# Kernel tuning notes

Hardware: AMD Instinct MI355X
Metric: run time of the kernel (lower is better)

Reference implementation:

```python
import jax, jax.numpy as jnp
import numpy as np

B, R, N, D, H, QK, K = 32, 200, 200, 128, 8, 16, 10
CLIP = 10.0  # standard POMO logit clipping


def setup_inputs() -> dict:
    key = jax.random.key(0)
    ks = jax.random.split(key, 12)
    encoded_nodes = jax.random.normal(ks[0], (B, N, D), jnp.float32)
    distance = jax.random.uniform(ks[1], (B, N, N), jnp.float32)
    current = jax.random.randint(ks[2], (B, R), 0, N)
    u = jax.random.uniform(ks[3], (B, R, N))
    ninf_mask = jnp.where(u < 0.3, -jnp.inf, 0.0).astype(jnp.float32)
    s = 0.02
    Wq = jax.random.normal(ks[4], (2 * D, H * QK), jnp.float32) * s
    Wk = jax.random.normal(ks[5], (D, H * QK), jnp.float32) * s
    Wv = jax.random.normal(ks[6], (D, H * QK), jnp.float32) * s
    Wmhc = jax.random.normal(ks[7], (H * QK, D), jnp.float32) * s
    b_mhc = jnp.zeros((D,), jnp.float32)
    W1 = jax.random.normal(ks[8], (K * D, 5 * D), jnp.float32) * s
    b1 = jnp.zeros((5 * D,), jnp.float32)
    W2 = jax.random.normal(ks[9], (5 * D, D), jnp.float32) * s
    b2 = jnp.zeros((D,), jnp.float32)
    return {"encoded_nodes": encoded_nodes, "distance": distance, "ninf_mask": ninf_mask,
            "current": current, "Wq": Wq, "Wk": Wk, "Wv": Wv, "Wmhc": Wmhc, "b_mhc": b_mhc,
            "W1": W1, "b1": b1, "W2": W2, "b2": b2}


def _search_unvisited(current, distance, ninf_mask):
    # rows of distance at current nodes: [B,R,N] (avoids B*R*N*N materialization)
    dist_f = jnp.take_along_axis(distance, current[:, :, None], axis=1)
    dist_m = jnp.where(jnp.isfinite(ninf_mask), dist_f, jnp.inf)
    neg_vals, idx = jax.lax.top_k(-dist_m, K)  # k smallest distances
    vals = -neg_vals
    return jnp.where(jnp.isinf(vals), N, idx)  # pad index N for masked-out slots


def _gather_pad0(encoded_nodes, idx):
    padded = jnp.concatenate([encoded_nodes, jnp.zeros((B, 1, D), encoded_nodes.dtype)], axis=1)
    g = jnp.take_along_axis(padded, idx.reshape(B, R * K)[:, :, None], axis=1)
    return g.reshape(B, R, K, D)


def _gather_pad_avg(a):
    # replace all-zero (pad) rows by the mean of non-zero rows within each [K,D] group
    is_zero = jnp.sum(a, axis=-1) == 0  # [B,R,K]
    cnt = jnp.maximum(jnp.sum(~is_zero, axis=-1).astype(a.dtype), 1e-9)  # [B,R]
    mean = jnp.sum(a, axis=2) / cnt[..., None]  # [B,R,D]
    return jnp.where(is_zero[..., None], mean[:, :, None, :], a)


def reference(encoded_nodes, distance, ninf_mask, current,
              Wq, Wk, Wv, Wmhc, b_mhc, W1, b1, W2, b2):
    knn = _search_unvisited(current, distance, ninf_mask)         # [B,R,K]
    a = _gather_pad0(encoded_nodes, knn)                          # [B,R,K,D]
    b = _gather_pad_avg(a)                                        # [B,R,K,D]
    h = jnp.maximum(b.reshape(B, R, K * D) @ W1 + b1, 0.0)
    unv = h @ W2 + b2                                             # [B,R,D]
    cur_emb = jnp.take_along_axis(encoded_nodes, current[:, :, None], axis=1)  # [B,R,D]
    qin = jnp.concatenate([cur_emb, unv], axis=-1)                # [B,R,2D]
    q = (qin @ Wq).reshape(B, R, H, QK).transpose(0, 2, 1, 3)     # [B,H,R,QK]
    k = (encoded_nodes @ Wk).reshape(B, N, H, QK).transpose(0, 2, 1, 3)
    v = (encoded_nodes @ Wv).reshape(B, N, H, QK).transpose(0, 2, 1, 3)
    score = jnp.einsum('bhrd,bhnd->bhrn', q, k) / jnp.sqrt(jnp.float32(QK))
    score = score + ninf_mask[:, None]                            # [B,H,R,N]
    w = jax.nn.softmax(score, axis=-1)
    out = jnp.einsum('bhrn,bhnd->bhrd', w, v)
    out = out.transpose(0, 2, 1, 3).reshape(B, R, H * QK)
    mh = out @ Wmhc + b_mhc                                       # [B,R,D]
    sh = jnp.einsum('brd,bnd->brn', mh, encoded_nodes) / jnp.sqrt(jnp.float32(D))
    logits = CLIP * jnp.tanh(sh) + ninf_mask
    return jax.nn.softmax(logits, axis=-1)                        # [B,R,N]
```

## Files before the change

kernel.cpp:

```cpp
#include <hip/hip_runtime.h>
#include <hip/hip_bf16.h>
#include <math.h>

#define Bc 32
#define Rc 200
#define Nc 200
#define Dc 128
#define Hc 8
#define QKc 16
#define Kc 10
#define BRc (Bc*Rc)

typedef __attribute__((ext_vector_type(8))) short short8;
typedef __attribute__((ext_vector_type(4))) float f32x4;
typedef unsigned long long u64;

#define GLOAD_LDS16(g, l) __builtin_amdgcn_global_load_lds( \
    (const __attribute__((address_space(1))) void*)(g), \
    (__attribute__((address_space(3))) void*)(l), 16, 0, 0)

__device__ inline void transpose_tile(const float* __restrict__ src, int lds_,
                                      __hip_bfloat16* __restrict__ dst, int ldd,
                                      int k0, int n0, float scale)
{
    __shared__ float tile[32][33];
    int tx = threadIdx.x & 31, ty = threadIdx.x >> 5;
    #pragma unroll
    for (int i = ty; i < 32; i += 8)
        tile[i][tx] = src[(size_t)(k0 + i) * lds_ + n0 + tx];
    __syncthreads();
    #pragma unroll
    for (int i = ty; i < 32; i += 8)
        dst[(size_t)(n0 + i) * ldd + k0 + tx] = __float2bfloat16(tile[tx][i] * scale);
}

__global__ __launch_bounds__(256) void prep_knn_kernel(
    const float* __restrict__ W1, const float* __restrict__ W2,
    const float* __restrict__ Wq, const float* __restrict__ Wmhc,
    const float* __restrict__ Wk, const float* __restrict__ Wv,
    const float* __restrict__ b2, const float* __restrict__ enc,
    const float* __restrict__ dist, const float* __restrict__ mask,
    const int* __restrict__ cur,
    __hip_bfloat16* __restrict__ W1t, __hip_bfloat16* __restrict__ Wkvt,
    __hip_bfloat16* __restrict__ Wmb, __hip_bfloat16* __restrict__ Wcat,
    float* __restrict__ bq, __hip_bfloat16* __restrict__ encb,
    unsigned* __restrict__ aoff, __hip_bfloat16* __restrict__ hq,
    u64* __restrict__ maskbits)
{
    int bid = blockIdx.x;
    int t = threadIdx.x;
    if (bid < 800) {
        transpose_tile(W1, 640, W1t, 1280, (bid % 40) * 32, (bid / 40) * 32, 1.f);
    } else if (bid < 816) {
        int id = bid - 800;
        transpose_tile(Wk, 128, Wkvt, 128, (id & 3) * 32, (id >> 2) * 32, 1.f);
    } else if (bid < 832) {
        int id = bid - 816;
        transpose_tile(Wv, 128, Wkvt + 128 * 128, 128, (id & 3) * 32, (id >> 2) * 32, 1.f);
    } else if (bid < 848) {
        int e = (bid - 832) * 1024 + t * 4;
        #pragma unroll
        for (int j = 0; j < 4; ++j) Wmb[e + j] = __float2bfloat16(Wmhc[e + j]);
    } else if (bid < 864) {
        int id = bid - 848;
        transpose_tile(Wq, 128, Wcat, 768, (id & 3) * 32, (id >> 2) * 32, 0.25f);
    } else if (bid < 904) {
        __shared__ float w2s[16 * 128];
        int j0 = (bid - 864) * 16;
        #pragma unroll
        for (int idx = t; idx < 16 * 128; idx += 256)
            w2s[idx] = W2[(size_t)j0 * 128 + idx];
        __syncthreads();
        int n = t & 127, half = t >> 7;
        float acc[8];
        #pragma unroll
        for (int jj = 0; jj < 8; ++jj) acc[jj] = 0.f;
        const float* wqp = Wq + (size_t)128 * 128 + n;
        #pragma unroll 8
        for (int k = 0; k < 128; ++k) {
            float wq = wqp[(size_t)k * 128];
            #pragma unroll
            for (int jj = 0; jj < 8; ++jj)
                acc[jj] = fmaf(w2s[(half * 8 + jj) * 128 + k], wq, acc[jj]);
        }
        #pragma unroll
        for (int jj = 0; jj < 8; ++jj)
            Wcat[(size_t)n * 768 + 128 + j0 + half * 8 + jj] =
                __float2bfloat16(acc[jj] * 0.25f);
    } else if (bid < 929) {
        size_t base = (size_t)(bid - 904) * 32768 + (size_t)t * 4;
        #pragma unroll 4
        for (int it = 0; it < 32; ++it) {
            size_t i = base + (size_t)it * 1024;
            float4 v = *(const float4*)(enc + i);
            encb[i + 0] = __float2bfloat16(v.x);
            encb[i + 1] = __float2bfloat16(v.y);
            encb[i + 2] = __float2bfloat16(v.z);
            encb[i + 3] = __float2bfloat16(v.w);
        }
    } else if (bid == 929) {
        __shared__ float red[128];
        int n = t & 127, half = t >> 7;
        float a0 = 0.f, a1 = 0.f;
        int kb = half * 64;
        #pragma unroll 8
        for (int k = 0; k < 64; k += 2) {
            a0 = fmaf(b2[kb + k],     Wq[(size_t)(128 + kb + k) * 128 + n], a0);
            a1 = fmaf(b2[kb + k + 1], Wq[(size_t)(128 + kb + k + 1) * 128 + n], a1);
        }
        if (half) red[n] = a0 + a1;
        __syncthreads();
        if (!half) bq[n] = (a0 + a1 + red[n]) * 0.25f;
    } else {
        int lane = t & 63, w = t >> 6;
        int br = (bid - 930) * 4 + w;
        int b = br / Rc;
        int c = cur[br];
        const float* drow = dist + ((size_t)b * Nc + c) * Nc;
        const float* mrow = mask + (size_t)br * Nc;

        float v[4];
        #pragma unroll
        for (int j = 0; j < 4; ++j) {
            int n = lane + 64 * j;
            bool allowed = false;
            float val = INFINITY;
            if (n < Nc) {
                float mv = mrow[n];
                if (!isinf(mv)) { val = drow[n]; allowed = true; }
            }
            v[j] = val;
            u64 wb = __ballot(allowed);
            if (lane == 0) maskbits[(size_t)br * 4 + j] = wb;
        }
        int idxs[Kc];
        unsigned myrow = 0;
        #pragma unroll
        for (int k = 0; k < Kc; ++k) {
            float bv = v[0]; int bn = lane;
            #pragma unroll
            for (int j = 1; j < 4; ++j) {
                if (v[j] < bv) { bv = v[j]; bn = lane + 64 * j; }
            }
            #pragma unroll
            for (int off = 32; off > 0; off >>= 1) {
                float ov = __shfl_xor(bv, off);
                int   on = __shfl_xor(bn, off);
                if (ov < bv || (ov == bv && on < bn)) { bv = ov; bn = on; }
            }
            bool pad = isinf(bv);
            idxs[k] = pad ? Nc : bn;
            if (lane == k) myrow = pad ? (unsigned)(Bc * Nc + br) : (unsigned)(b * Nc + bn);
            int oj = bn >> 6, ol = bn & 63;
            if (!pad && lane == ol) v[oj] = INFINITY;
        }
        if (lane < Kc) aoff[(size_t)br * 16 + lane] = myrow << 7;

        const float* erow = enc + ((size_t)b * Nc + c) * Dc;
        __hip_bfloat16* hrow = hq + (size_t)br * 768;
        hrow[lane]      = __float2bfloat16(erow[lane]);
        hrow[lane + 64] = __float2bfloat16(erow[lane + 64]);

        if (idxs[Kc - 1] == Nc) {
            float cnt = 0.f;
            #pragma unroll
            for (int k = 0; k < Kc; ++k) cnt += (idxs[k] < Nc) ? 1.f : 0.f;
            float icnt = 1.f / fmaxf(cnt, 1e-9f);
            #pragma unroll
            for (int half = 0; half < 2; ++half) {
                int d = lane + 64 * half;
                float sum = 0.f;
                #pragma unroll
                for (int k = 0; k < Kc; ++k) {
                    if (idxs[k] < Nc)
                        sum += enc[((size_t)b * Nc + idxs[k]) * Dc + d];
                }
                encb[((size_t)(Bc * Nc) + br) * Dc + d] = __float2bfloat16(sum * icnt);
            }
        }
    }
}

__global__ __launch_bounds__(256) void fused_gemms_kernel(
    const __hip_bfloat16* __restrict__ encb, const unsigned* __restrict__ aoff,
    const __hip_bfloat16* __restrict__ W1t, const float* __restrict__ b1,
    const __hip_bfloat16* __restrict__ Wkvt, const __hip_bfloat16* __restrict__ Wmb,
    const float* __restrict__ bmhc, const float* __restrict__ enc,
    __hip_bfloat16* __restrict__ hq, __hip_bfloat16* __restrict__ kvf,
    __hip_bfloat16* __restrict__ em, float* __restrict__ be)
{
    __shared__ short Asl[4][64 * 32];
    __shared__ short Bsl[4][64 * 32];
    int bid = blockIdx.x;
    int tid = threadIdx.x;
    int wave = tid >> 6, lane = tid & 63;
    int lrow = lane >> 2;
    int cg   = lane & 3;
    int ss   = (lane >> 3) & 3;
    int gq   = (cg - ss) & 3;
    int wm = wave >> 1, wn = wave & 1;
    int rrow = lane & 15, quad = lane >> 4;
    int srd  = (rrow >> 1) & 3;
    int strip = (wave & 1) * 32;

    if (bid < 1000) {
        int m0 = (bid / 10) * 64, n0 = (bid % 10) * 64;
        unsigned o0[Kc], o1[Kc];
        if (wave < 2) {
            const unsigned* ap0 = aoff + (size_t)(m0 + strip + lrow) * 16;
            const unsigned* ap1 = ap0 + 16 * 16;
            #pragma unroll
            for (int j = 0; j < Kc; ++j) { o0[j] = ap0[j]; o1[j] = ap1[j]; }
        }
        const short* Eb = (const short*)encb;
        const short* gB0 = (const short*)W1t + (size_t)(n0 + strip + lrow) * 1280 + gq * 8;
        const short* gB1 = gB0 + (size_t)16 * 1280;

        f32x4 acc[2][2];
        #pragma unroll
        for (int i = 0; i < 2; ++i)
            #pragma unroll
            for (int j = 0; j < 2; ++j)
                acc[i][j] = (f32x4){0.f, 0.f, 0.f, 0.f};

        #pragma unroll
        for (int kt = 0; kt < 10; ++kt) {
            __syncthreads();
            #pragma unroll
            for (int s = 0; s < 4; ++s) {
                if (wave < 2) {
                    GLOAD_LDS16(Eb + o0[kt] + s * 32 + gq * 8, &Asl[s][strip * 32]);
                    GLOAD_LDS16(Eb + o1[kt] + s * 32 + gq * 8, &Asl[s][(strip + 16) * 32]);
                } else {
                    GLOAD_LDS16(gB0 + kt * 128 + s * 32, &Bsl[s][strip * 32]);
                    GLOAD_LDS16(gB1 + kt * 128 + s * 32, &Bsl[s][(strip + 16) * 32]);
                }
            }
            __syncthreads();
            #pragma unroll
            for (int s = 0; s < 4; ++s) {
                short8 afr[2], bfr[2];
                #pragma unroll
                for (int mt = 0; mt < 2; ++mt)
                    afr[mt] = *(const short8*)&Asl[s][(wm * 32 + mt * 16 + rrow) * 32 + ((quad + srd) & 3) * 8];
                #pragma unroll
                for (int nt = 0; nt < 2; ++nt)
                    bfr[nt] = *(const short8*)&Bsl[s][(wn * 32 + nt * 16 + rrow) * 32 + ((quad + srd) & 3) * 8];
                #pragma unroll
                for (int mt = 0; mt < 2; ++mt)
                    #pragma unroll
                    for (int nt = 0; nt < 2; ++nt)
                        acc[mt][nt] = __builtin_amdgcn_mfma_f32_16x16x32_bf16(
                            afr[mt], bfr[nt], acc[mt][nt], 0, 0, 0);
            }
        }
        #pragma unroll
        for (int mt = 0; mt < 2; ++mt)
            #pragma unroll
            for (int nt = 0; nt < 2; ++nt) {
                int n = wn * 32 + nt * 16 + rrow;
                float bv = b1[n0 + n];
                #pragma unroll
                for (int i = 0; i < 4; ++i) {
                    int m = m0 + wm * 32 + mt * 16 + quad * 4 + i;
                    float vv = fmaxf(acc[mt][nt][i] + bv, 0.f);
                    hq[(size_t)m * 768 + 128 + n0 + n] = __float2bfloat16(vv);
                }
            }
    } else if (bid < 1600) {
        const short* Bbase; __hip_bfloat16* Cout; int ldc, m0, n0;
        if (bid < 1400) {
            int id = bid - 1000;
            Bbase = (const short*)Wkvt; Cout = kvf; ldc = 256;
            m0 = (id >> 2) * 64; n0 = (id & 3) * 64;
        } else {
            int id = bid - 1400;
            Bbase = (const short*)Wmb; Cout = em; ldc = 128;
            m0 = (id >> 1) * 64; n0 = (id & 1) * 64;
        }
        const short* g0 = (wave < 2)
            ? (const short*)encb + (size_t)(m0 + strip + lrow) * 128 + gq * 8
            : Bbase + (size_t)(n0 + strip + lrow) * 128 + gq * 8;
        const short* g1 = g0 + (size_t)16 * 128;

        f32x4 acc[2][2];
        #pragma unroll
        for (int i = 0; i < 2; ++i)
            #pragma unroll
            for (int j = 0; j < 2; ++j)
                acc[i][j] = (f32x4){0.f, 0.f, 0.f, 0.f};

        #pragma unroll
        for (int s = 0; s < 4; ++s) {
            short* l0 = (wave < 2) ? &Asl[s][strip * 32] : &Bsl[s][strip * 32];
            short* l1 = (wave < 2) ? &Asl[s][(strip + 16) * 32] : &Bsl[s][(strip + 16) * 32];
            GLOAD_LDS16(g0 + s * 32, l0);
            GLOAD_LDS16(g1 + s * 32, l1);
        }
        __syncthreads();
        #pragma unroll
        for (int s = 0; s < 4; ++s) {
            short8 afr[2], bfr[2];
            #pragma unroll
            for (int mt = 0; mt < 2; ++mt)
                afr[mt] = *(const short8*)&Asl[s][(wm * 32 + mt * 16 + rrow) * 32 + ((quad + srd) & 3) * 8];
            #pragma unroll
            for (int nt = 0; nt < 2; ++nt)
                bfr[nt] = *(const short8*)&Bsl[s][(wn * 32 + nt * 16 + rrow) * 32 + ((quad + srd) & 3) * 8];
            #pragma unroll
            for (int mt = 0; mt < 2; ++mt)
                #pragma unroll
                for (int nt = 0; nt < 2; ++nt)
                    acc[mt][nt] = __builtin_amdgcn_mfma_f32_16x16x32_bf16(
                        afr[mt], bfr[nt], acc[mt][nt], 0, 0, 0);
        }
        #pragma unroll
        for (int mt = 0; mt < 2; ++mt)
            #pragma unroll
            for (int nt = 0; nt < 2; ++nt) {
                int n = wn * 32 + nt * 16 + rrow;
                #pragma unroll
                for (int i = 0; i < 4; ++i) {
                    int m = m0 + wm * 32 + mt * 16 + quad * 4 + i;
                    Cout[(size_t)m * ldc + n0 + n] = __float2bfloat16(acc[mt][nt][i]);
                }
            }
    } else {
        int i = (bid - 1600) * 256 + tid;
        if (i < Bc * Nc) {
            const float* row = enc + (size_t)i * 128;
            float acc = 0.f;
            #pragma unroll
            for (int dq = 0; dq < 32; ++dq) {
                float4 e4 = *(const float4*)(row + dq * 4);
                acc = fmaf(bmhc[dq * 4 + 0], e4.x, acc);
                acc = fmaf(bmhc[dq * 4 + 1], e4.y, acc);
                acc = fmaf(bmhc[dq * 4 + 2], e4.z, acc);
                acc = fmaf(bmhc[dq * 4 + 3], e4.w, acc);
            }
            be[i] = acc;
        }
    }
}

__global__ __launch_bounds__(256) void qgemm_kernel(
    const __hip_bfloat16* __restrict__ hq, const __hip_bfloat16* __restrict__ Wcat,
    const float* __restrict__ bq, __hip_bfloat16* __restrict__ q)
{
    __shared__ short Asl[4][64 * 32];
    __shared__ short Bsl[4][64 * 32];
    int tid = threadIdx.x;
    int wave = tid >> 6, lane = tid & 63;
    int m0 = blockIdx.y * 64, n0 = blockIdx.x * 64;
    int lrow = lane >> 2;
    int cg   = lane & 3;
    int ss   = (lane >> 3) & 3;
    int gq   = (cg - ss) & 3;
    int wm = wave >> 1, wn = wave & 1;
    int rrow = lane & 15, quad = lane >> 4;
    int srd  = (rrow >> 1) & 3;
    int strip = (wave & 1) * 32;

    const short* g0 = (wave < 2)
        ? (const short*)hq + (size_t)(m0 + strip + lrow) * 768 + gq * 8
        : (const short*)Wcat + (size_t)(n0 + strip + lrow) * 768 + gq * 8;
    const short* g1 = g0 + (size_t)16 * 768;

    f32x4 acc[2][2];
    #pragma unroll
    for (int i = 0; i < 2; ++i)
        #pragma unroll
        for (int j = 0; j < 2; ++j)
            acc[i][j] = (f32x4){0.f, 0.f, 0.f, 0.f};

    for (int k0 = 0; k0 < 768; k0 += 128) {
        __syncthreads();
        #pragma unroll
        for (int s = 0; s < 4; ++s) {
            short* l0 = (wave < 2) ? &Asl[s][strip * 32] : &Bsl[s][strip * 32];
            short* l1 = (wave < 2) ? &Asl[s][(strip + 16) * 32] : &Bsl[s][(strip + 16) * 32];
            GLOAD_LDS16(g0 + k0 + s * 32, l0);
            GLOAD_LDS16(g1 + k0 + s * 32, l1);
        }
        __syncthreads();
        #pragma unroll
        for (int s = 0; s < 4; ++s) {
            short8 afr[2], bfr[2];
            #pragma unroll
            for (int mt = 0; mt < 2; ++mt)
                afr[mt] = *(const short8*)&Asl[s][(wm * 32 + mt * 16 + rrow) * 32 + ((quad + srd) & 3) * 8];
            #pragma unroll
            for (int nt = 0; nt < 2; ++nt)
                bfr[nt] = *(const short8*)&Bsl[s][(wn * 32 + nt * 16 + rrow) * 32 + ((quad + srd) & 3) * 8];
            #pragma unroll
            for (int mt = 0; mt < 2; ++mt)
                #pragma unroll
                for (int nt = 0; nt < 2; ++nt)
                    acc[mt][nt] = __builtin_amdgcn_mfma_f32_16x16x32_bf16(
                        afr[mt], bfr[nt], acc[mt][nt], 0, 0, 0);
        }
    }

    #pragma unroll
    for (int mt = 0; mt < 2; ++mt) {
        #pragma unroll
        for (int nt = 0; nt < 2; ++nt) {
            int n = wn * 32 + nt * 16 + rrow;
            float bv = bq[n0 + n];
            #pragma unroll
            for (int i = 0; i < 4; ++i) {
                int m = m0 + wm * 32 + mt * 16 + quad * 4 + i;
                q[(size_t)m * 128 + n0 + n] = __float2bfloat16(acc[mt][nt][i] + bv);
            }
        }
    }
}

__global__ __launch_bounds__(256) void attn_mfma_kernel(
    const __hip_bfloat16* __restrict__ q, const __hip_bfloat16* __restrict__ kvf,
    const u64* __restrict__ maskbits, __hip_bfloat16* __restrict__ att)
{
    constexpr int RP = 208;
    constexpr int QS = 40;
    constexpr int VS = 232;
    __shared__ short Qs[RP * QS];
    __shared__ short Ks[RP * QS];
    __shared__ short Vt[16 * VS];
    __shared__ short Ps[4][16 * VS];
    __shared__ u64 smask[RP][4];

    int b = blockIdx.x >> 3, h = blockIdx.x & 7;
    int half = blockIdx.y;
    int t = threadIdx.x;
    int wave = t >> 6, lane = t & 63;
    int rrow = lane & 15, quad = lane >> 4;

    const short8 z8 = {0, 0, 0, 0, 0, 0, 0, 0};
    for (int idx = t; idx < RP * 2; idx += 256) {
        int r = idx >> 1, g = idx & 1;
        short8 qa = z8, ka = z8;
        if (r < Rc) {
            qa = *(const short8*)((const short*)q + ((size_t)(b * Rc + r)) * 128 + h * 16 + g * 8);
            ka = *(const short8*)((const short*)kvf + ((size_t)(b * Nc + r)) * 256 + h * 16 + g * 8);
        }
        *(short8*)&Qs[r * QS + g * 8] = qa;
        *(short8*)&Ks[r * QS + g * 8] = ka;
        *(short8*)&Qs[r * QS + 16 + g * 8] = z8;
        *(short8*)&Ks[r * QS + 16 + g * 8] = z8;
    }
    if (t < Rc) {
        const short* vp = (const short*)kvf + ((size_t)(b * Nc + t)) * 256 + 128 + h * 16;
        short8 v0 = *(const short8*)vp;
        short8 v1 = *(const short8*)(vp + 8);
        #pragma unroll
        for (int d = 0; d < 8; ++d) Vt[d * VS + t] = v0[d];
        #pragma unroll
        for (int d = 0; d < 8; ++d) Vt[(d + 8) * VS + t] = v1[d];
    }
    for (int idx = t; idx < 16 * 32; idx += 256) {
        int d = idx >> 5, cN = 200 + (idx & 31);
        if (cN < VS) Vt[d * VS + cN] = 0;
    }
    for (int idx = lane; idx < 16 * 16; idx += 64) {
        int rr = idx >> 4, cc = 208 + (idx & 15);
        Ps[wave][rr * VS + cc] = 0;
    }
    for (int idx = t; idx < RP * 4; idx += 256) {
        int r = idx >> 2, w = idx & 3;
        smask[r][w] = (r < Rc) ? maskbits[((size_t)b * Rc + r) * 4 + w] : ~0ull;
    }
    __syncthreads();

    int rt0 = half * 7, rt1 = half ? 13 : 7;
    for (int rt = rt0 + wave; rt < rt1; rt += 4) {
        short8 qf = *(const short8*)&Qs[(rt * 16 + rrow) * QS + quad * 8];
        f32x4 sacc[13];
        #pragma unroll
        for (int nt = 0; nt < 13; ++nt) {
            short8 kf = *(const short8*)&Ks[(nt * 16 + rrow) * QS + quad * 8];
            sacc[nt] = __builtin_amdgcn_mfma_f32_16x16x32_bf16(
                qf, kf, (f32x4){0.f, 0.f, 0.f, 0.f}, 0, 0, 0);
        }
        float inv[4];
        #pragma unroll
        for (int i = 0; i < 4; ++i) {
            int r = rt * 16 + quad * 4 + i;
            u64 wv0 = smask[r][0], wv1 = smask[r][1], wv2 = smask[r][2], wv3 = smask[r][3];
            float mx = -INFINITY;
            #pragma unroll
            for (int nt = 0; nt < 13; ++nt) {
                u64 w = (nt < 4) ? wv0 : (nt < 8) ? wv1 : (nt < 12) ? wv2 : wv3;
                int sh = ((nt & 3) << 4) + rrow;
                float s = ((w >> sh) & 1ull) ? sacc[nt][i] : -INFINITY;
                sacc[nt][i] = s;
                mx = fmaxf(mx, s);
            }
            mx = fmaxf(mx, __shfl_xor(mx, 1));
            mx = fmaxf(mx, __shfl_xor(mx, 2));
            mx = fmaxf(mx, __shfl_xor(mx, 4));
            mx = fmaxf(mx, __shfl_xor(mx, 8));
            float l = 0.f;
            #pragma unroll
            for (int nt = 0; nt < 13; ++nt) {
                float p = __expf(sacc[nt][i] - mx);
                sacc[nt][i] = p;
                l += p;
            }
            l += __shfl_xor(l, 1);
            l += __shfl_xor(l, 2);
            l += __shfl_xor(l, 4);
            l += __shfl_xor(l, 8);
            inv[i] = (l > 0.f) ? 1.f / l : 0.f;
        }
        #pragma unroll
        for (int nt = 0; nt < 13; ++nt)
            #pragma unroll
            for (int i = 0; i < 4; ++i)
                *(__hip_bfloat16*)&Ps[wave][(quad * 4 + i) * VS + nt * 16 + rrow] =
                    __float2bfloat16(sacc[nt][i]);
        f32x4 oacc = (f32x4){0.f, 0.f, 0.f, 0.f};
        #pragma unroll
        for (int kt = 0; kt < 7; ++kt) {
            short8 pf = *(const short8*)&Ps[wave][rrow * VS + kt * 32 + quad * 8];
            short8 vf = *(const short8*)&Vt[rrow * VS + kt * 32 + quad * 8];
            oacc = __builtin_amdgcn_mfma_f32_16x16x32_bf16(pf, vf, oacc, 0, 0, 0);
        }
        #pragma unroll
        for (int i = 0; i < 4; ++i) {
            int r = rt * 16 + quad * 4 + i;
            if (r < Rc)
                att[((size_t)(b * Rc + r)) * 128 + h * 16 + rrow] =
                    __float2bfloat16(oacc[i] * inv[i]);
        }
    }
}

__global__ __launch_bounds__(128) void logits_softmax_kernel(
    const __hip_bfloat16* __restrict__ att, const __hip_bfloat16* __restrict__ em,
    const float* __restrict__ be, const u64* __restrict__ maskbits,
    float* __restrict__ out)
{
    __shared__ short Asl[4][32 * 32];
    __shared__ short Bsl[4][208 * 32];
    __shared__ u64 sm[32][4];
    __shared__ float sbe[208];
    int b = blockIdx.x, m0 = blockIdx.y * 32;
    int t = threadIdx.x, wave = t >> 6, lane = t & 63;
    int lrow = lane >> 2, cg = lane & 3, ss = (lane >> 3) & 3, gq = (cg - ss) & 3;
    int rrow = lane & 15, quad = lane >> 4, srd = (rrow >> 1) & 3;

    const short* Aa = (const short*)att + ((size_t)b * Rc + m0) * 128;
    const short* Ben = (const short*)em + (size_t)b * Nc * 128;

    #pragma unroll
    for (int kc = 0; kc < 4; ++kc)
        GLOAD_LDS16(Aa + (size_t)(wave * 16 + lrow) * 128 + kc * 32 + gq * 8,
                    &Asl[kc][(wave * 16) * 32]);
    for (int cch = wave; cch < 13; cch += 2)
        #pragma unroll
        for (int kc = 0; kc < 4; ++kc)
            GLOAD_LDS16(Ben + (size_t)(cch * 16 + lrow) * 128 + kc * 32 + gq * 8,
                        &Bsl[kc][(cch * 16) * 32]);
    {
        int r = t >> 2, w = t & 3;
        sm[r][w] = (m0 + r < Rc) ? maskbits[((size_t)b * Rc + m0 + r) * 4 + w] : 0ull;
    }
    for (int i = t; i < 208; i += 128) sbe[i] = (i < Nc) ? be[(size_t)b * Nc + i] : 0.f;
    __syncthreads();

    short8 afr[4];
    #pragma unroll
    for (int kc = 0; kc < 4; ++kc)
        afr[kc] = *(const short8*)&Asl[kc][(wave * 16 + rrow) * 32 + ((quad + srd) & 3) * 8];

    f32x4 acc[13];
    #pragma unroll
    for (int nt = 0; nt < 13; ++nt)
        acc[nt] = (f32x4){0.f, 0.f, 0.f, 0.f};
    #pragma unroll
    for (int nt = 0; nt < 13; ++nt)
        #pragma unroll
        for (int kc = 0; kc < 4; ++kc) {
            short8 bfr = *(const short8*)
                &Bsl[kc][(nt * 16 + rrow) * 32 + ((quad + srd) & 3) * 8];
            acc[nt] = __builtin_amdgcn_mfma_f32_16x16x32_bf16(afr[kc], bfr, acc[nt], 0, 0, 0);
        }

    const float scale = 0.08838834764831843f;
    #pragma unroll
    for (int i = 0; i < 4; ++i) {
        int rloc = wave * 16 + quad * 4 + i;
        int r = m0 + rloc;
        u64 w0 = sm[rloc][0], w1 = sm[rloc][1], w2 = sm[rloc][2], w3 = sm[rloc][3];
        float vals[13];
        float mx = -INFINITY;
        #pragma unroll
        for (int nt = 0; nt < 13; ++nt) {
            u64 w = (nt < 4) ? w0 : (nt < 8) ? w1 : (nt < 12) ? w2 : w3;
            int sh = ((nt & 3) << 4) + rrow;
            float lg = ((w >> sh) & 1ull)
                     ? 10.f * tanhf((acc[nt][i] + sbe[nt * 16 + rrow]) * scale)
                     : -INFINITY;
            vals[nt] = lg;
            mx = fmaxf(mx, lg);
        }
        mx = fmaxf(mx, __shfl_xor(mx, 1));
        mx = fmaxf(mx, __shfl_xor(mx, 2));
        mx = fmaxf(mx, __shfl_xor(mx, 4));
        mx = fmaxf(mx, __shfl_xor(mx, 8));
        float l = 0.f;
        #pragma unroll
        for (int nt = 0; nt < 13; ++nt) {
            float p = (vals[nt] == -INFINITY) ? 0.f : __expf(vals[nt] - mx);
            vals[nt] = p;
            l += p;
        }
        l += __shfl_xor(l, 1);
        l += __shfl_xor(l, 2);
        l += __shfl_xor(l, 4);
        l += __shfl_xor(l, 8);
        float inv = (l > 0.f) ? 1.f / l : 0.f;
        if (r < Rc) {
            #pragma unroll
            for (int nt = 0; nt < 13; ++nt) {
                int n = nt * 16 + rrow;
                if (n < Nc)
                    out[((size_t)b * Rc + r) * Nc + n] = vals[nt] * inv;
            }
        }
    }
}

extern "C" void kernel_launch(void* const* d_in, const int* in_sizes, int n_in,
                              void* d_out, int out_size, void* d_ws, size_t ws_size,
                              hipStream_t stream)
{
    const float* enc  = (const float*)d_in[0];
    const float* dist = (const float*)d_in[1];
    const float* mask = (const float*)d_in[2];
    const int*   cur  = (const int*)d_in[3];
    const float* Wq   = (const float*)d_in[4];
    const float* Wk   = (const float*)d_in[5];
    const float* Wv   = (const float*)d_in[6];
    const float* Wmhc = (const float*)d_in[7];
    const float* bmhc = (const float*)d_in[8];
    const float* W1   = (const float*)d_in[9];
    const float* b1   = (const float*)d_in[10];
    const float* W2   = (const float*)d_in[11];
    const float* b2   = (const float*)d_in[12];
    float* out = (float*)d_out;

    char* ws = (char*)d_ws;
    size_t off = 0;
    auto alloc = [&](size_t bytes) { char* p = ws + off; off += (bytes + 255) & ~(size_t)255; return p; };
    __hip_bfloat16* W1t  = (__hip_bfloat16*)alloc((size_t)640 * 1280 * 2);
    __hip_bfloat16* Wkvt = (__hip_bfloat16*)alloc((size_t)256 * 128 * 2);
    __hip_bfloat16* Wmb  = (__hip_bfloat16*)alloc((size_t)128 * 128 * 2);
    __hip_bfloat16* Wcat = (__hip_bfloat16*)alloc((size_t)128 * 768 * 2);
    float* bq = (float*)alloc((size_t)128 * 4);
    __hip_bfloat16* encb = (__hip_bfloat16*)alloc((size_t)(Bc * Nc + BRc + 64) * Dc * 2);
    unsigned* aoff = (unsigned*)alloc((size_t)BRc * 16 * 4);
    __hip_bfloat16* hq   = (__hip_bfloat16*)alloc((size_t)BRc * 768 * 2);
    __hip_bfloat16* q    = (__hip_bfloat16*)alloc((size_t)BRc * 128 * 2);
    __hip_bfloat16* kvf  = (__hip_bfloat16*)alloc((size_t)Bc * Nc * 256 * 2);
    __hip_bfloat16* att  = (__hip_bfloat16*)alloc((size_t)(BRc + 64) * 128 * 2);
    __hip_bfloat16* em   = (__hip_bfloat16*)alloc((size_t)(Bc * Nc + 64) * 128 * 2);
    float* be = (float*)alloc((size_t)Bc * Nc * 4);
    u64* maskbits = (u64*)alloc((size_t)BRc * 4 * 8);

    prep_knn_kernel<<<2530, 256, 0, stream>>>(
        W1, W2, Wq, Wmhc, Wk, Wv, b2, enc, dist, mask, cur,
        W1t, Wkvt, Wmb, Wcat, bq, encb, aoff, hq, maskbits);
    fused_gemms_kernel<<<1625, 256, 0, stream>>>(
        encb, aoff, W1t, b1, Wkvt, Wmb, bmhc, enc, hq, kvf, em, be);
    qgemm_kernel<<<dim3(2, BRc / 64), 256, 0, stream>>>(hq, Wcat, bq, q);
    attn_mfma_kernel<<<dim3(Bc * Hc, 2), 256, 0, stream>>>(q, kvf, maskbits, att);
    logits_softmax_kernel<<<dim3(Bc, 7), 128, 0, stream>>>(att, em, be, maskbits, out);
}
```

Baseline: 163.7 us.

## Fuse five kernel launches into one persistent kernel with grid barriers

The five stage kernels are merged into one persistent mega kernel launched with a fixed grid of 512 blocks. Each stage walks its original block indices in a grid-stride loop, and stages are separated by a software grid barrier built on an atomic counter, which is reset by a memset before the launch. The aim is to remove launch gaps and tail idle time between stages. In exchange it relies on all 512 blocks being co-resident, and it uses a large static shared-memory buffer that may limit occupancy. The barrier also has a spin timeout that could silently break correctness.

Result: slower. 441.1 us (+169.4%).

```diff
diff --git a/kernel.cpp b/kernel.cpp
--- a/kernel.cpp
+++ b/kernel.cpp
@@ -10,6 +10,7 @@
 #define QKc 16
 #define Kc 10
 #define BRc (Bc*Rc)
+#define GRID 512
 
 typedef __attribute__((ext_vector_type(8))) short short8;
 typedef __attribute__((ext_vector_type(4))) float f32x4;
@@ -19,222 +20,365 @@
     (const __attribute__((address_space(1))) void*)(g), \
     (__attribute__((address_space(3))) void*)(l), 16, 0, 0)
 
-__device__ inline void transpose_tile(const float* __restrict__ src, int lds_,
-                                      __hip_bfloat16* __restrict__ dst, int ldd,
-                                      int k0, int n0, float scale)
+__device__ __forceinline__ void grid_sync(unsigned* bar, unsigned target)
 {
-    __shared__ float tile[32][33];
+    __syncthreads();
+    if (threadIdx.x == 0) {
+        __threadfence();
+        __hip_atomic_fetch_add(bar, 1u, __ATOMIC_ACQ_REL, __HIP_MEMORY_SCOPE_AGENT);
+        unsigned spins = 0;
+        while (__hip_atomic_load(bar, __ATOMIC_ACQUIRE, __HIP_MEMORY_SCOPE_AGENT) < target) {
+            __builtin_amdgcn_s_sleep(2);
+            if (++spins > 10000000u) break;
+        }
+    }
+    __syncthreads();
+}
+
+__device__ __forceinline__ void transpose_tile2(float* tile ,
+    const float* __restrict__ src, int lds_, __hip_bfloat16* __restrict__ dst,
+    int ldd, int k0, int n0, float scale)
+{
     int tx = threadIdx.x & 31, ty = threadIdx.x >> 5;
     #pragma unroll
     for (int i = ty; i < 32; i += 8)
-        tile[i][tx] = src[(size_t)(k0 + i) * lds_ + n0 + tx];
+        tile[i * 33 + tx] = src[(size_t)(k0 + i) * lds_ + n0 + tx];
     __syncthreads();
     #pragma unroll
     for (int i = ty; i < 32; i += 8)
-        dst[(size_t)(n0 + i) * ldd + k0 + tx] = __float2bfloat16(tile[tx][i] * scale);
+        dst[(size_t)(n0 + i) * ldd + k0 + tx] = __float2bfloat16(tile[tx * 33 + i] * scale);
 }
 
-__global__ __launch_bounds__(256) void prep_knn_kernel(
+__global__ __launch_bounds__(256, 2) void mega_kernel(
     const float* __restrict__ W1, const float* __restrict__ W2,
     const float* __restrict__ Wq, const float* __restrict__ Wmhc,
     const float* __restrict__ Wk, const float* __restrict__ Wv,
+    const float* __restrict__ bmhc, const float* __restrict__ b1,
     const float* __restrict__ b2, const float* __restrict__ enc,
-    const float* __restrict__ dist, const float* __restrict__ mask,
+    const float* __restrict__ dist, const float* __restrict__ maskp,
     const int* __restrict__ cur,
     __hip_bfloat16* __restrict__ W1t, __hip_bfloat16* __restrict__ Wkvt,
     __hip_bfloat16* __restrict__ Wmb, __hip_bfloat16* __restrict__ Wcat,
     float* __restrict__ bq, __hip_bfloat16* __restrict__ encb,
     unsigned* __restrict__ aoff, __hip_bfloat16* __restrict__ hq,
-    u64* __restrict__ maskbits)
+    __hip_bfloat16* __restrict__ q, __hip_bfloat16* __restrict__ kvf,
+    __hip_bfloat16* __restrict__ att, __hip_bfloat16* __restrict__ em,
+    float* __restrict__ be, u64* __restrict__ maskbits,
+    float* __restrict__ out, unsigned* __restrict__ bar)
 {
-    int bid = blockIdx.x;
+    __shared__ __align__(16) char SMEM[78336];
     int t = threadIdx.x;
-    if (bid < 800) {
-        transpose_tile(W1, 640, W1t, 1280, (bid % 40) * 32, (bid / 40) * 32, 1.f);
-    } else if (bid < 816) {
-        int id = bid - 800;
-        transpose_tile(Wk, 128, Wkvt, 128, (id & 3) * 32, (id >> 2) * 32, 1.f);
-    } else if (bid < 832) {
-        int id = bid - 816;
-        transpose_tile(Wv, 128, Wkvt + 128 * 128, 128, (id & 3) * 32, (id >> 2) * 32, 1.f);
-    } else if (bid < 848) {
-        int e = (bid - 832) * 1024 + t * 4;
-        #pragma unroll
-        for (int j = 0; j < 4; ++j) Wmb[e + j] = __float2bfloat16(Wmhc[e + j]);
-    } else if (bid < 864) {
-        int id = bid - 848;
-        transpose_tile(Wq, 128, Wcat, 768, (id & 3) * 32, (id >> 2) * 32, 0.25f);
-    } else if (bid < 904) {
-        __shared__ float w2s[16 * 128];
-        int j0 = (bid - 864) * 16;
-        #pragma unroll
-        for (int idx = t; idx < 16 * 128; idx += 256)
-            w2s[idx] = W2[(size_t)j0 * 128 + idx];
+    int wave = t >> 6, lane = t & 63;
+    int lrow = lane >> 2, cg = lane & 3, ss = (lane >> 3) & 3, gq = (cg - ss) & 3;
+    int wm = wave >> 1, wn = wave & 1;
+    int rrow = lane & 15, quad = lane >> 4, srd = (rrow >> 1) & 3;
+    int strip = (wave & 1) * 32;
+
+    for (int j = blockIdx.x; j < 2530; j += GRID) {
+        if (j < 800) {
+            transpose_tile2((float*)SMEM, W1, 640, W1t, 1280, (j % 40) * 32, (j / 40) * 32, 1.f);
+        } else if (j < 816) {
+            int id = j - 800;
+            transpose_tile2((float*)SMEM, Wk, 128, Wkvt, 128, (id & 3) * 32, (id >> 2) * 32, 1.f);
+        } else if (j < 832) {
+            int id = j - 816;
+            transpose_tile2((float*)SMEM, Wv, 128, Wkvt + 128 * 128, 128, (id & 3) * 32, (id >> 2) * 32, 1.f);
+        } else if (j < 848) {
+            int e = (j - 832) * 1024 + t * 4;
+            #pragma unroll
+            for (int jj = 0; jj < 4; ++jj) Wmb[e + jj] = __float2bfloat16(Wmhc[e + jj]);
+        } else if (j < 864) {
+            int id = j - 848;
+            transpose_tile2((float*)SMEM, Wq, 128, Wcat, 768, (id & 3) * 32, (id >> 2) * 32, 0.25f);
+        } else if (j < 904) {
+            float* w2s = (float*)SMEM;
+            int j0 = (j - 864) * 16;
+            for (int idx = t; idx < 16 * 128; idx += 256)
+                w2s[idx] = W2[(size_t)j0 * 128 + idx];
+            __syncthreads();
+            int n = t & 127, half = t >> 7;
+            float acc[8];
+            #pragma unroll
+            for (int jj = 0; jj < 8; ++jj) acc[jj] = 0.f;
+            const float* wqp = Wq + (size_t)128 * 128 + n;
+            #pragma unroll 8
+            for (int k = 0; k < 128; ++k) {
+                float wq = wqp[(size_t)k * 128];
+                #pragma unroll
+                for (int jj = 0; jj < 8; ++jj)
+                    acc[jj] = fmaf(w2s[(half * 8 + jj) * 128 + k], wq, acc[jj]);
+            }
+            #pragma unroll
+            for (int jj = 0; jj < 8; ++jj)
+                Wcat[(size_t)n * 768 + 128 + j0 + half * 8 + jj] =
+                    __float2bfloat16(acc[jj] * 0.25f);
+        } else if (j < 929) {
+            size_t base = (size_t)(j - 904) * 32768 + (size_t)t * 4;
+            #pragma unroll 4
+            for (int it = 0; it < 32; ++it) {
+                size_t i = base + (size_t)it * 1024;
+                float4 v = *(const float4*)(enc + i);
+                encb[i + 0] = __float2bfloat16(v.x);
+                encb[i + 1] = __float2bfloat16(v.y);
+                encb[i + 2] = __float2bfloat16(v.z);
+                encb[i + 3] = __float2bfloat16(v.w);
+            }
+        } else if (j == 929) {
+            float* red = (float*)SMEM;
+            int n = t & 127, half = t >> 7;
+            float a0 = 0.f, a1 = 0.f;
+            int kb = half * 64;
+            #pragma unroll 8
+            for (int k = 0; k < 64; k += 2) {
+                a0 = fmaf(b2[kb + k],     Wq[(size_t)(128 + kb + k) * 128 + n], a0);
+                a1 = fmaf(b2[kb + k + 1], Wq[(size_t)(128 + kb + k + 1) * 128 + n], a1);
+            }
+            if (half) red[n] = a0 + a1;
+            __syncthreads();
+            if (!half) bq[n] = (a0 + a1 + red[n]) * 0.25f;
+        } else {
+            int br = (j - 930) * 4 + wave;
+            int b = br / Rc;
+            int c = cur[br];
+            const float* drow = dist + ((size_t)b * Nc + c) * Nc;
+            const float* mrow = maskp + (size_t)br * Nc;
+
+            float v[4];
+            #pragma unroll
+            for (int jj = 0; jj < 4; ++jj) {
+                int n = lane + 64 * jj;
+                bool allowed = false;
+                float val = INFINITY;
+                if (n < Nc) {
+                    float mv = mrow[n];
+                    if (!isinf(mv)) { val = drow[n]; allowed = true; }
+                }
+                v[jj] = val;
+                u64 wb = __ballot(allowed);
+                if (lane == 0) maskbits[(size_t)br * 4 + jj] = wb;
+            }
+            int idxs[Kc];
+            unsigned myrow = 0;
+            #pragma unroll
+            for (int k = 0; k < Kc; ++k) {
+                float bv = v[0]; int bn = lane;
+                #pragma unroll
+                for (int jj = 1; jj < 4; ++jj) {
+                    if (v[jj] < bv) { bv = v[jj]; bn = lane + 64 * jj; }
+                }
+                #pragma unroll
+                for (int off = 32; off > 0; off >>= 1) {
+                    float ov = __shfl_xor(bv, off);
+                    int   on = __shfl_xor(bn, off);
+                    if (ov < bv || (ov == bv && on < bn)) { bv = ov; bn = on; }
+                }
+                bool pad = isinf(bv);
+                idxs[k] = pad ? Nc : bn;
+                if (lane == k) myrow = pad ? (unsigned)(Bc * Nc + br) : (unsigned)(b * Nc + bn);
+                int oj = bn >> 6, ol = bn & 63;
+                if (!pad && lane == ol) v[oj] = INFINITY;
+            }
+            if (lane < Kc) aoff[(size_t)br * 16 + lane] = myrow << 7;
+
+            const float* erow = enc + ((size_t)b * Nc + c) * Dc;
+            __hip_bfloat16* hrow = hq + (size_t)br * 768;
+            hrow[lane]      = __float2bfloat16(erow[lane]);
+            hrow[lane + 64] = __float2bfloat16(erow[lane + 64]);
+
+            if (idxs[Kc - 1] == Nc) {
+                float cnt = 0.f;
+                #pragma unroll
+                for (int k = 0; k < Kc; ++k) cnt += (idxs[k] < Nc) ? 1.f : 0.f;
+                float icnt = 1.f / fmaxf(cnt, 1e-9f);
+                #pragma unroll
+                for (int half = 0; half < 2; ++half) {
+                    int d = lane + 64 * half;
+                    float sum = 0.f;
+                    #pragma unroll
+                    for (int k = 0; k < Kc; ++k) {
+                        if (idxs[k] < Nc)
+                            sum += enc[((size_t)b * Nc + idxs[k]) * Dc + d];
+                    }
+                    encb[((size_t)(Bc * Nc) + br) * Dc + d] = __float2bfloat16(sum * icnt);
+                }
+            }
+        }
         __syncthreads();
-        int n = t & 127, half = t >> 7;
-        float acc[8];
-        #pragma unroll
-        for (int jj = 0; jj < 8; ++jj) acc[jj] = 0.f;
-        const float* wqp = Wq + (size_t)128 * 128 + n;
-        #pragma unroll 8
-        for (int k = 0; k < 128; ++k) {
-            float wq = wqp[(size_t)k * 128];
-            #pragma unroll
-            for (int jj = 0; jj < 8; ++jj)
-                acc[jj] = fmaf(w2s[(half * 8 + jj) * 128 + k], wq, acc[jj]);
-        }
-        #pragma unroll
-        for (int jj = 0; jj < 8; ++jj)
-            Wcat[(size_t)n * 768 + 128 + j0 + half * 8 + jj] =
-                __float2bfloat16(acc[jj] * 0.25f);
-    } else if (bid < 929) {
-        size_t base = (size_t)(bid - 904) * 32768 + (size_t)t * 4;
-        #pragma unroll 4
-        for (int it = 0; it < 32; ++it) {
-            size_t i = base + (size_t)it * 1024;
-            float4 v = *(const float4*)(enc + i);
-            encb[i + 0] = __float2bfloat16(v.x);
-            encb[i + 1] = __float2bfloat16(v.y);
-            encb[i + 2] = __float2bfloat16(v.z);
-            encb[i + 3] = __float2bfloat16(v.w);
-        }
-    } else if (bid == 929) {
-        __shared__ float red[128];
-        int n = t & 127, half = t >> 7;
-        float a0 = 0.f, a1 = 0.f;
-        int kb = half * 64;
-        #pragma unroll 8
-        for (int k = 0; k < 64; k += 2) {
-            a0 = fmaf(b2[kb + k],     Wq[(size_t)(128 + kb + k) * 128 + n], a0);
-            a1 = fmaf(b2[kb + k + 1], Wq[(size_t)(128 + kb + k + 1) * 128 + n], a1);
-        }
-        if (half) red[n] = a0 + a1;
-        __syncthreads();
-        if (!half) bq[n] = (a0 + a1 + red[n]) * 0.25f;
-    } else {
-        int lane = t & 63, w = t >> 6;
-        int br = (bid - 930) * 4 + w;
-        int b = br / Rc;
-        int c = cur[br];
-        const float* drow = dist + ((size_t)b * Nc + c) * Nc;
-        const float* mrow = mask + (size_t)br * Nc;
-
-        float v[4];
-        #pragma unroll
-        for (int j = 0; j < 4; ++j) {
-            int n = lane + 64 * j;
-            bool allowed = false;
-            float val = INFINITY;
-            if (n < Nc) {
-                float mv = mrow[n];
-                if (!isinf(mv)) { val = drow[n]; allowed = true; }
-            }
-            v[j] = val;
-            u64 wb = __ballot(allowed);
-            if (lane == 0) maskbits[(size_t)br * 4 + j] = wb;
-        }
-        int idxs[Kc];
-        unsigned myrow = 0;
-        #pragma unroll
-        for (int k = 0; k < Kc; ++k) {
-            float bv = v[0]; int bn = lane;
-            #pragma unroll
-            for (int j = 1; j < 4; ++j) {
-                if (v[j] < bv) { bv = v[j]; bn = lane + 64 * j; }
-            }
-            #pragma unroll
-            for (int off = 32; off > 0; off >>= 1) {
-                float ov = __shfl_xor(bv, off);
-                int   on = __shfl_xor(bn, off);
-                if (ov < bv || (ov == bv && on < bn)) { bv = ov; bn = on; }
-            }
-            bool pad = isinf(bv);
-            idxs[k] = pad ? Nc : bn;
-            if (lane == k) myrow = pad ? (unsigned)(Bc * Nc + br) : (unsigned)(b * Nc + bn);
-            int oj = bn >> 6, ol = bn & 63;
-            if (!pad && lane == ol) v[oj] = INFINITY;
-        }
-        if (lane < Kc) aoff[(size_t)br * 16 + lane] = myrow << 7;
-
-        const float* erow = enc + ((size_t)b * Nc + c) * Dc;
-        __hip_bfloat16* hrow = hq + (size_t)br * 768;
-        hrow[lane]      = __float2bfloat16(erow[lane]);
-        hrow[lane + 64] = __float2bfloat16(erow[lane + 64]);
-
-        if (idxs[Kc - 1] == Nc) {
-            float cnt = 0.f;
-            #pragma unroll
-            for (int k = 0; k < Kc; ++k) cnt += (idxs[k] < Nc) ? 1.f : 0.f;
-            float icnt = 1.f / fmaxf(cnt, 1e-9f);
-            #pragma unroll
-            for (int half = 0; half < 2; ++half) {
-                int d = lane + 64 * half;
-                float sum = 0.f;
-                #pragma unroll
-                for (int k = 0; k < Kc; ++k) {
-                    if (idxs[k] < Nc)
-                        sum += enc[((size_t)b * Nc + idxs[k]) * Dc + d];
-                }
-                encb[((size_t)(Bc * Nc) + br) * Dc + d] = __float2bfloat16(sum * icnt);
-            }
-        }
     }
-}
-
-__global__ __launch_bounds__(256) void fused_gemms_kernel(
-    const __hip_bfloat16* __restrict__ encb, const unsigned* __restrict__ aoff,
-    const __hip_bfloat16* __restrict__ W1t, const float* __restrict__ b1,
-    const __hip_bfloat16* __restrict__ Wkvt, const __hip_bfloat16* __restrict__ Wmb,
-    const float* __restrict__ bmhc, const float* __restrict__ enc,
-    __hip_bfloat16* __restrict__ hq, __hip_bfloat16* __restrict__ kvf,
-    __hip_bfloat16* __restrict__ em, float* __restrict__ be)
-{
-    __shared__ short Asl[4][64 * 32];
-    __shared__ short Bsl[4][64 * 32];
-    int bid = blockIdx.x;
-    int tid = threadIdx.x;
-    int wave = tid >> 6, lane = tid & 63;
-    int lrow = lane >> 2;
-    int cg   = lane & 3;
-    int ss   = (lane >> 3) & 3;
-    int gq   = (cg - ss) & 3;
-    int wm = wave >> 1, wn = wave & 1;
-    int rrow = lane & 15, quad = lane >> 4;
-    int srd  = (rrow >> 1) & 3;
-    int strip = (wave & 1) * 32;
-
-    if (bid < 1000) {
-        int m0 = (bid / 10) * 64, n0 = (bid % 10) * 64;
-        unsigned o0[Kc], o1[Kc];
-        if (wave < 2) {
-            const unsigned* ap0 = aoff + (size_t)(m0 + strip + lrow) * 16;
-            const unsigned* ap1 = ap0 + 16 * 16;
-            #pragma unroll
-            for (int j = 0; j < Kc; ++j) { o0[j] = ap0[j]; o1[j] = ap1[j]; }
-        }
-        const short* Eb = (const short*)encb;
-        const short* gB0 = (const short*)W1t + (size_t)(n0 + strip + lrow) * 1280 + gq * 8;
-        const short* gB1 = gB0 + (size_t)16 * 1280;
+    grid_sync(bar, GRID);
+
+    {
+        short* Asl = (short*)SMEM;
+        short* Bsl = (short*)(SMEM + 16384);
+        for (int j = blockIdx.x; j < 1625; j += GRID) {
+            if (j < 1000) {
+                int m0 = (j / 10) * 64, n0 = (j % 10) * 64;
+                unsigned o0[Kc], o1[Kc];
+                if (wave < 2) {
+                    const unsigned* ap0 = aoff + (size_t)(m0 + strip + lrow) * 16;
+                    const unsigned* ap1 = ap0 + 16 * 16;
+                    #pragma unroll
+                    for (int jj = 0; jj < Kc; ++jj) { o0[jj] = ap0[jj]; o1[jj] = ap1[jj]; }
+                }
+                const short* Eb = (const short*)encb;
+                const short* gB0 = (const short*)W1t + (size_t)(n0 + strip + lrow) * 1280 + gq * 8;
+                const short* gB1 = gB0 + (size_t)16 * 1280;
+
+                f32x4 acc[2][2];
+                #pragma unroll
+                for (int i = 0; i < 2; ++i)
+                    #pragma unroll
+                    for (int jj = 0; jj < 2; ++jj)
+                        acc[i][jj] = (f32x4){0.f, 0.f, 0.f, 0.f};
+
+                #pragma unroll
+                for (int kt = 0; kt < 10; ++kt) {
+                    __syncthreads();
+                    #pragma unroll
+                    for (int s = 0; s < 4; ++s) {
+                        if (wave < 2) {
+                            GLOAD_LDS16(Eb + o0[kt] + s * 32 + gq * 8, Asl + s * 2048 + strip * 32);
+                            GLOAD_LDS16(Eb + o1[kt] + s * 32 + gq * 8, Asl + s * 2048 + (strip + 16) * 32);
+                        } else {
+                            GLOAD_LDS16(gB0 + kt * 128 + s * 32, Bsl + s * 2048 + strip * 32);
+                            GLOAD_LDS16(gB1 + kt * 128 + s * 32, Bsl + s * 2048 + (strip + 16) * 32);
+                        }
+                    }
+                    __syncthreads();
+                    #pragma unroll
+                    for (int s = 0; s < 4; ++s) {
+                        short8 afr[2], bfr[2];
+                        #pragma unroll
+                        for (int mt = 0; mt < 2; ++mt)
+                            afr[mt] = *(const short8*)(Asl + s * 2048 + (wm * 32 + mt * 16 + rrow) * 32 + ((quad + srd) & 3) * 8);
+                        #pragma unroll
+                        for (int nt = 0; nt < 2; ++nt)
+                            bfr[nt] = *(const short8*)(Bsl + s * 2048 + (wn * 32 + nt * 16 + rrow) * 32 + ((quad + srd) & 3) * 8);
+                        #pragma unroll
+                        for (int mt = 0; mt < 2; ++mt)
+                            #pragma unroll
+                            for (int nt = 0; nt < 2; ++nt)
+                                acc[mt][nt] = __builtin_amdgcn_mfma_f32_16x16x32_bf16(
+                                    afr[mt], bfr[nt], acc[mt][nt], 0, 0, 0);
+                    }
+                }
+                #pragma unroll
+                for (int mt = 0; mt < 2; ++mt)
+                    #pragma unroll
+                    for (int nt = 0; nt < 2; ++nt) {
+                        int n = wn * 32 + nt * 16 + rrow;
+                        float bv = b1[n0 + n];
+                        #pragma unroll
+                        for (int i = 0; i < 4; ++i) {
+                            int m = m0 + wm * 32 + mt * 16 + quad * 4 + i;
+                            float vv = fmaxf(acc[mt][nt][i] + bv, 0.f);
+                            hq[(size_t)m * 768 + 128 + n0 + n] = __float2bfloat16(vv);
+                        }
+                    }
+            } else if (j < 1600) {
+                const short* Bbase; __hip_bfloat16* Cout; int ldc, m0, n0;
+                if (j < 1400) {
+                    int id = j - 1000;
+                    Bbase = (const short*)Wkvt; Cout = kvf; ldc = 256;
+                    m0 = (id >> 2) * 64; n0 = (id & 3) * 64;
+                } else {
+                    int id = j - 1400;
+                    Bbase = (const short*)Wmb; Cout = em; ldc = 128;
+                    m0 = (id >> 1) * 64; n0 = (id & 1) * 64;
+                }
+                const short* g0 = (wave < 2)
+                    ? (const short*)encb + (size_t)(m0 + strip + lrow) * 128 + gq * 8
+                    : Bbase + (size_t)(n0 + strip + lrow) * 128 + gq * 8;
+                const short* g1 = g0 + (size_t)16 * 128;
+
+                f32x4 acc[2][2];
+                #pragma unroll
+                for (int i = 0; i < 2; ++i)
+                    #pragma unroll
+                    for (int jj = 0; jj < 2; ++jj)
+                        acc[i][jj] = (f32x4){0.f, 0.f, 0.f, 0.f};
+
+                __syncthreads();
+                #pragma unroll
+                for (int s = 0; s < 4; ++s) {
+                    short* l0 = (wave < 2) ? (Asl + s * 2048 + strip * 32) : (Bsl + s * 2048 + strip * 32);
+                    short* l1 = (wave < 2) ? (Asl + s * 2048 + (strip + 16) * 32) : (Bsl + s * 2048 + (strip + 16) * 32);
+                    GLOAD_LDS16(g0 + s * 32, l0);
+                    GLOAD_LDS16(g1 + s * 32, l1);
+                }
+                __syncthreads();
+                #pragma unroll
+                for (int s = 0; s < 4; ++s) {
+                    short8 afr[2], bfr[2];
+                    #pragma unroll
+                    for (int mt = 0; mt < 2; ++mt)
+                        afr[mt] = *(const short8*)(Asl + s * 2048 + (wm * 32 + mt * 16 + rrow) * 32 + ((quad + srd) & 3) * 8);
+                    #pragma unroll
+                    for (int nt = 0; nt < 2; ++nt)
+                        bfr[nt] = *(const short8*)(Bsl + s * 2048 + (wn * 32 + nt * 16 + rrow) * 32 + ((quad + srd) & 3) * 8);
+                    #pragma unroll
+                    for (int mt = 0; mt < 2; ++mt)
+                        #pragma unroll
+                        for (int nt = 0; nt < 2; ++nt)
+                            acc[mt][nt] = __builtin_amdgcn_mfma_f32_16x16x32_bf16(
+                                afr[mt], bfr[nt], acc[mt][nt], 0, 0, 0);
+                }
+                #pragma unroll
+                for (int mt = 0; mt < 2; ++mt)
+                    #pragma unroll
+                    for (int nt = 0; nt < 2; ++nt) {
+                        int n = wn * 32 + nt * 16 + rrow;
+                        #pragma unroll
+                        for (int i = 0; i < 4; ++i) {
+                            int m = m0 + wm * 32 + mt * 16 + quad * 4 + i;
+                            Cout[(size_t)m * ldc + n0 + n] = __float2bfloat16(acc[mt][nt][i]);
+                        }
+                    }
+            } else {
+                int i = (j - 1600) * 256 + t;
+                if (i < Bc * Nc) {
+                    const float* row = enc + (size_t)i * 128;
+                    float acc = 0.f;
+                    #pragma unroll
+                    for (int dq = 0; dq < 32; ++dq) {
+                        float4 e4 = *(const float4*)(row + dq * 4);
+                        acc = fmaf(bmhc[dq * 4 + 0], e4.x, acc);
+                        acc = fmaf(bmhc[dq * 4 + 1], e4.y, acc);
+                        acc = fmaf(bmhc[dq * 4 + 2], e4.z, acc);
+                        acc = fmaf(bmhc[dq * 4 + 3], e4.w, acc);
+                    }
+                    be[i] = acc;
+                }
+            }
+        }
+    }
+    grid_sync(bar, 2 * GRID);
+
+    if (blockIdx.x < 200) {
+        short* Asl = (short*)SMEM;
+        short* Bsl = (short*)(SMEM + 16384);
+        int m0 = (blockIdx.x >> 1) * 64, n0 = (blockIdx.x & 1) * 64;
+
+        const short* g0 = (wave < 2)
+            ? (const short*)hq + (size_t)(m0 + strip + lrow) * 768 + gq * 8
+            : (const short*)Wcat + (size_t)(n0 + strip + lrow) * 768 + gq * 8;
+        const short* g1 = g0 + (size_t)16 * 768;
 
         f32x4 acc[2][2];
         #pragma unroll
         for (int i = 0; i < 2; ++i)
             #pragma unroll
-            for (int j = 0; j < 2; ++j)
-                acc[i][j] = (f32x4){0.f, 0.f, 0.f, 0.f};
-
-        #pragma unroll
-        for (int kt = 0; kt < 10; ++kt) {
+            for (int jj = 0; jj < 2; ++jj)
+                acc[i][jj] = (f32x4){0.f, 0.f, 0.f, 0.f};
+
+        for (int k0 = 0; k0 < 768; k0 += 128) {
             __syncthreads();
             #pragma unroll
             for (int s = 0; s < 4; ++s) {
-                if (wave < 2) {
-                    GLOAD_LDS16(Eb + o0[kt] + s * 32 + gq * 8, &Asl[s][strip * 32]);
-                    GLOAD_LDS16(Eb + o1[kt] + s * 32 + gq * 8, &Asl[s][(strip + 16) * 32]);
-                } else {
-                    GLOAD_LDS16(gB0 + kt * 128 + s * 32, &Bsl[s][strip * 32]);
-                    GLOAD_LDS16(gB1 + kt * 128 + s * 32, &Bsl[s][(strip + 16) * 32]);
-                }
+                short* l0 = (wave < 2) ? (Asl + s * 2048 + strip * 32) : (Bsl + s * 2048 + strip * 32);
+                short* l1 = (wave < 2) ? (Asl + s * 2048 + (strip + 16) * 32) : (Bsl + s * 2048 + (strip + 16) * 32);
+                GLOAD_LDS16(g0 + k0 + s * 32, l0);
+                GLOAD_LDS16(g1 + k0 + s * 32, l1);
             }
             __syncthreads();
             #pragma unroll
@@ -242,10 +386,10 @@
                 short8 afr[2], bfr[2];
                 #pragma unroll
                 for (int mt = 0; mt < 2; ++mt)
-                    afr[mt] = *(const short8*)&Asl[s][(wm * 32 + mt * 16 + rrow) * 32 + ((quad + srd) & 3) * 8];
+                    afr[mt] = *(const short8*)(Asl + s * 2048 + (wm * 32 + mt * 16 + rrow) * 32 + ((quad + srd) & 3) * 8);
                 #pragma unroll
                 for (int nt = 0; nt < 2; ++nt)
-                    bfr[nt] = *(const short8*)&Bsl[s][(wn * 32 + nt * 16 + rrow) * 32 + ((quad + srd) & 3) * 8];
+                    bfr[nt] = *(const short8*)(Bsl + s * 2048 + (wn * 32 + nt * 16 + rrow) * 32 + ((quad + srd) & 3) * 8);
                 #pragma unroll
                 for (int mt = 0; mt < 2; ++mt)
                     #pragma unroll
@@ -259,241 +403,195 @@
             #pragma unroll
             for (int nt = 0; nt < 2; ++nt) {
                 int n = wn * 32 + nt * 16 + rrow;
-                float bv = b1[n0 + n];
+                float bv = bq[n0 + n];
                 #pragma unroll
                 for (int i = 0; i < 4; ++i) {
                     int m = m0 + wm * 32 + mt * 16 + quad * 4 + i;
-                    float vv = fmaxf(acc[mt][nt][i] + bv, 0.f);
-                    hq[(size_t)m * 768 + 128 + n0 + n] = __float2bfloat16(vv);
-                }
-            }
-    } else if (bid < 1600) {
-        const short* Bbase; __hip_bfloat16* Cout; int ldc, m0, n0;
-        if (bid < 1400) {
-            int id = bid - 1000;
-            Bbase = (const short*)Wkvt; Cout = kvf; ldc = 256;
-            m0 = (id >> 2) * 64; n0 = (id & 3) * 64;
-        } else {
-            int id = bid - 1400;
-            Bbase = (const short*)Wmb; Cout = em; ldc = 128;
-            m0 = (id >> 1) * 64; n0 = (id & 1) * 64;
-        }
-        const short* g0 = (wave < 2)
-            ? (const short*)encb + (size_t)(m0 + strip + lrow) * 128 + gq * 8
-            : Bbase + (size_t)(n0 + strip + lrow) * 128 + gq * 8;
-        const short* g1 = g0 + (size_t)16 * 128;
-
-        f32x4 acc[2][2];
+                    q[(size_t)m * 128 + n0 + n] = __float2bfloat16(acc[mt][nt][i] + bv);
+                }
+            }
+    }
+    grid_sync(bar, 3 * GRID);
+
+    {
+        constexpr int RP = 208;
+        constexpr int QS = 40;
+        constexpr int VS = 232;
+        short* Qs = (short*)SMEM;
+        short* Ks = (short*)(SMEM + 16640);
+        short* Vt = (short*)(SMEM + 33280);
+        short* Ps = (short*)(SMEM + 40704);
+        u64*  smask = (u64*)(SMEM + 70400);
+
+        int jb = blockIdx.x;
+        int half = jb & 1, h = (jb >> 1) & 7, b = jb >> 4;
+        short* PsW = Ps + wave * (16 * VS);
+
+        const short8 z8 = {0, 0, 0, 0, 0, 0, 0, 0};
+        for (int idx = t; idx < RP * 2; idx += 256) {
+            int r = idx >> 1, g = idx & 1;
+            short8 qa = z8, ka = z8;
+            if (r < Rc) {
+                qa = *(const short8*)((const short*)q + ((size_t)(b * Rc + r)) * 128 + h * 16 + g * 8);
+                ka = *(const short8*)((const short*)kvf + ((size_t)(b * Nc + r)) * 256 + h * 16 + g * 8);
+            }
+            *(short8*)&Qs[r * QS + g * 8] = qa;
+            *(short8*)&Ks[r * QS + g * 8] = ka;
+            *(short8*)&Qs[r * QS + 16 + g * 8] = z8;
+            *(short8*)&Ks[r * QS + 16 + g * 8] = z8;
+        }
+        if (t < Rc) {
+            const short* vp = (const short*)kvf + ((size_t)(b * Nc + t)) * 256 + 128 + h * 16;
+            short8 v0 = *(const short8*)vp;
+            short8 v1 = *(const short8*)(vp + 8);
+            #pragma unroll
+            for (int d = 0; d < 8; ++d) Vt[d * VS + t] = v0[d];
+            #pragma unroll
+            for (int d = 0; d < 8; ++d) Vt[(d + 8) * VS + t] = v1[d];
+        }
+        for (int idx = t; idx < 16 * 32; idx += 256) {
+            int d = idx >> 5, cN = 200 + (idx & 31);
+            if (cN < VS) Vt[d * VS + cN] = 0;
+        }
+        for (int idx = lane; idx < 16 * 16; idx += 64) {
+            int rr = idx >> 4, cc = 208 + (idx & 15);
+            PsW[rr * VS + cc] = 0;
+        }
+        for (int idx = t; idx < RP * 4; idx += 256) {
+            int r = idx >> 2, w = idx & 3;
+            smask[r * 4 + w] = (r < Rc) ? maskbits[((size_t)b * Rc + r) * 4 + w] : ~0ull;
+        }
+        __syncthreads();
+
+        int rt0 = half * 7, rt1 = half ? 13 : 7;
+        for (int rt = rt0 + wave; rt < rt1; rt += 4) {
+            short8 qf = *(const short8*)&Qs[(rt * 16 + rrow) * QS + quad * 8];
+            f32x4 sacc[13];
+            #pragma unroll
+            for (int nt = 0; nt < 13; ++nt) {
+                short8 kf = *(const short8*)&Ks[(nt * 16 + rrow) * QS + quad * 8];
+                sacc[nt] = __builtin_amdgcn_mfma_f32_16x16x32_bf16(
+                    qf, kf, (f32x4){0.f, 0.f, 0.f, 0.f}, 0, 0, 0);
+            }
+            float inv[4];
+            #pragma unroll
+            for (int i = 0; i < 4; ++i) {
+                int r = rt * 16 + quad * 4 + i;
+                u64 wv0 = smask[r * 4 + 0], wv1 = smask[r * 4 + 1];
+                u64 wv2 = smask[r * 4 + 2], wv3 = smask[r * 4 + 3];
+                float mx = -INFINITY;
+                #pragma unroll
+                for (int nt = 0; nt < 13; ++nt) {
+                    u64 w = (nt < 4) ? wv0 : (nt < 8) ? wv1 : (nt < 12) ? wv2 : wv3;
+                    int sh = ((nt & 3) << 4) + rrow;
+                    float s = ((w >> sh) & 1ull) ? sacc[nt][i] : -INFINITY;
+                    sacc[nt][i] = s;
+                    mx = fmaxf(mx, s);
+                }
+                mx = fmaxf(mx, __shfl_xor(mx, 1));
+                mx = fmaxf(mx, __shfl_xor(mx, 2));
+                mx = fmaxf(mx, __shfl_xor(mx, 4));
+                mx = fmaxf(mx, __shfl_xor(mx, 8));
+                float l = 0.f;
+                #pragma unroll
+                for (int nt = 0; nt < 13; ++nt) {
+                    float p = __expf(sacc[nt][i] - mx);
+                    sacc[nt][i] = p;
+                    l += p;
+                }
+                l += __shfl_xor(l, 1);
+                l += __shfl_xor(l, 2);
+                l += __shfl_xor(l, 4);
+                l += __shfl_xor(l, 8);
+                inv[i] = (l > 0.f) ? 1.f / l : 0.f;
+            }
+            #pragma unroll
+            for (int nt = 0; nt < 13; ++nt)
+                #pragma unroll
+                for (int i = 0; i < 4; ++i)
+                    *(__hip_bfloat16*)&PsW[(quad * 4 + i) * VS + nt * 16 + rrow] =
+                        __float2bfloat16(sacc[nt][i]);
+            f32x4 oacc = (f32x4){0.f, 0.f, 0.f, 0.f};
+            #pragma unroll
+            for (int kt = 0; kt < 7; ++kt) {
+                short8 pf = *(const short8*)&PsW[rrow * VS + kt * 32 + quad * 8];
+                short8 vf = *(const short8*)&Vt[rrow * VS + kt * 32 + quad * 8];
+                oacc = __builtin_amdgcn_mfma_f32_16x16x32_bf16(pf, vf, oacc, 0, 0, 0);
+            }
+            #pragma unroll
+            for (int i = 0; i < 4; ++i) {
+                int r = rt * 16 + quad * 4 + i;
+                if (r < Rc)
+                    att[((size_t)(b * Rc + r)) * 128 + h * 16 + rrow] =
+                        __float2bfloat16(oacc[i] * inv[i]);
+            }
+        }
+    }
+    grid_sync(bar, 4 * GRID);
+
+    if (blockIdx.x < 128) {
+        short* Asl = (short*)SMEM;
+        short* Bsl = (short*)(SMEM + 16384);
+        u64*  sm  = (u64*)(SMEM + 69632);
+        float* sbe = (float*)(SMEM + 71680);
+
+        int b = blockIdx.x >> 2, m0 = (blockIdx.x & 3) * 64;
+
+        const short* Aa = (const short*)att + ((size_t)b * Rc + m0) * 128;
+        const short* Ben = (const short*)em + (size_t)b * Nc * 128;
+
         #pragma unroll
-        for (int i = 0; i < 2; ++i)
-            #pragma unroll
-            for (int j = 0; j < 2; ++j)
-                acc[i][j] = (f32x4){0.f, 0.f, 0.f, 0.f};
-
+        for (int kc = 0; kc < 4; ++kc)
+            GLOAD_LDS16(Aa + (size_t)(wave * 16 + lrow) * 128 + kc * 32 + gq * 8,
+                        Asl + kc * 2048 + (wave * 16) * 32);
+        for (int cch = wave; cch < 13; cch += 4)
+            #pragma unroll
+            for (int kc = 0; kc < 4; ++kc)
+                GLOAD_LDS16(Ben + (size_t)(cch * 16 + lrow) * 128 + kc * 32 + gq * 8,
+                            Bsl + kc * 208 * 32 + (cch * 16) * 32);
+        {
+            int r = t >> 2, w = t & 3;
+            sm[r * 4 + w] = (m0 + r < Rc) ? maskbits[((size_t)b * Rc + m0 + r) * 4 + w] : 0ull;
+        }
+        if (t < 208) sbe[t] = (t < Nc) ? be[(size_t)b * Nc + t] : 0.f;
+        __syncthreads();
+
+        short8 afr[4];
         #pragma unroll
-        for (int s = 0; s < 4; ++s) {
-            short* l0 = (wave < 2) ? &Asl[s][strip * 32] : &Bsl[s][strip * 32];
-            short* l1 = (wave < 2) ? &Asl[s][(strip + 16) * 32] : &Bsl[s][(strip + 16) * 32];
-            GLOAD_LDS16(g0 + s * 32, l0);
-            GLOAD_LDS16(g1 + s * 32, l1);
-        }
-        __syncthreads();
+        for (int kc = 0; kc < 4; ++kc)
+            afr[kc] = *(const short8*)(Asl + kc * 2048 + (wave * 16 + rrow) * 32 + ((quad + srd) & 3) * 8);
+
+        f32x4 acc[13];
         #pragma unroll
-        for (int s = 0; s < 4; ++s) {
-            short8 afr[2], bfr[2];
-            #pragma unroll
-            for (int mt = 0; mt < 2; ++mt)
-                afr[mt] = *(const short8*)&Asl[s][(wm * 32 + mt * 16 + rrow) * 32 + ((quad + srd) & 3) * 8];
-            #pragma unroll
-            for (int nt = 0; nt < 2; ++nt)
-                bfr[nt] = *(const short8*)&Bsl[s][(wn * 32 + nt * 16 + rrow) * 32 + ((quad + srd) & 3) * 8];
-            #pragma unroll
-            for (int mt = 0; mt < 2; ++mt)
-                #pragma unroll
-                for (int nt = 0; nt < 2; ++nt)
-                    acc[mt][nt] = __builtin_amdgcn_mfma_f32_16x16x32_bf16(
-                        afr[mt], bfr[nt], acc[mt][nt], 0, 0, 0);
-        }
+        for (int nt = 0; nt < 13; ++nt)
+            acc[nt] = (f32x4){0.f, 0.f, 0.f, 0.f};
         #pragma unroll
-        for (int mt = 0; mt < 2; ++mt)
-            #pragma unroll
-            for (int nt = 0; nt < 2; ++nt) {
-                int n = wn * 32 + nt * 16 + rrow;
-                #pragma unroll
-                for (int i = 0; i < 4; ++i) {
-                    int m = m0 + wm * 32 + mt * 16 + quad * 4 + i;
-                    Cout[(size_t)m * ldc + n0 + n] = __float2bfloat16(acc[mt][nt][i]);
-                }
-            }
-    } else {
-        int i = (bid - 1600) * 256 + tid;
-        if (i < Bc * Nc) {
-            const float* row = enc + (size_t)i * 128;
-            float acc = 0.f;
-            #pragma unroll
-            for (int dq = 0; dq < 32; ++dq) {
-                float4 e4 = *(const float4*)(row + dq * 4);
-                acc = fmaf(bmhc[dq * 4 + 0], e4.x, acc);
-                acc = fmaf(bmhc[dq * 4 + 1], e4.y, acc);
-                acc = fmaf(bmhc[dq * 4 + 2], e4.z, acc);
-                acc = fmaf(bmhc[dq * 4 + 3], e4.w, acc);
-            }
-            be[i] = acc;
-        }
-    }
-}
-
-__global__ __launch_bounds__(256) void qgemm_kernel(
-    const __hip_bfloat16* __restrict__ hq, const __hip_bfloat16* __restrict__ Wcat,
-    const float* __restrict__ bq, __hip_bfloat16* __restrict__ q)
-{
-    __shared__ short Asl[4][64 * 32];
-    __shared__ short Bsl[4][64 * 32];
-    int tid = threadIdx.x;
-    int wave = tid >> 6, lane = tid & 63;
-    int m0 = blockIdx.y * 64, n0 = blockIdx.x * 64;
-    int lrow = lane >> 2;
-    int cg   = lane & 3;
-    int ss   = (lane >> 3) & 3;
-    int gq   = (cg - ss) & 3;
-    int wm = wave >> 1, wn = wave & 1;
-    int rrow = lane & 15, quad = lane >> 4;
-    int srd  = (rrow >> 1) & 3;
-    int strip = (wave & 1) * 32;
-
-    const short* g0 = (wave < 2)
-        ? (const short*)hq + (size_t)(m0 + strip + lrow) * 768 + gq * 8
-        : (const short*)Wcat + (size_t)(n0 + strip + lrow) * 768 + gq * 8;
-    const short* g1 = g0 + (size_t)16 * 768;
-
-    f32x4 acc[2][2];
-    #pragma unroll
-    for (int i = 0; i < 2; ++i)
-        #pragma unroll
-        for (int j = 0; j < 2; ++j)
-            acc[i][j] = (f32x4){0.f, 0.f, 0.f, 0.f};
-
-    for (int k0 = 0; k0 < 768; k0 += 128) {
-        __syncthreads();
-        #pragma unroll
-        for (int s = 0; s < 4; ++s) {
-            short* l0 = (wave < 2) ? &Asl[s][strip * 32] : &Bsl[s][strip * 32];
-            short* l1 = (wave < 2) ? &Asl[s][(strip + 16) * 32] : &Bsl[s][(strip + 16) * 32];
-            GLOAD_LDS16(g0 + k0 + s * 32, l0);
-            GLOAD_LDS16(g1 + k0 + s * 32, l1);
-        }
-        __syncthreads();
-        #pragma unroll
-        for (int s = 0; s < 4; ++s) {
-            short8 afr[2], bfr[2];
-            #pragma unroll
-            for (int mt = 0; mt < 2; ++mt)
-                afr[mt] = *(const short8*)&Asl[s][(wm * 32 + mt * 16 + rrow) * 32 + ((quad + srd) & 3) * 8];
-            #pragma unroll
-            for (int nt = 0; nt < 2; ++nt)
-                bfr[nt] = *(const short8*)&Bsl[s][(wn * 32 + nt * 16 + rrow) * 32 + ((quad + srd) & 3) * 8];
-            #pragma unroll
-            for (int mt = 0; mt < 2; ++mt)
-                #pragma unroll
-                for (int nt = 0; nt < 2; ++nt)
-                    acc[mt][nt] = __builtin_amdgcn_mfma_f32_16x16x32_bf16(
-                        afr[mt], bfr[nt], acc[mt][nt], 0, 0, 0);
-        }
-    }
-
-    #pragma unroll
-    for (int mt = 0; mt < 2; ++mt) {
-        #pragma unroll
-        for (int nt = 0; nt < 2; ++nt) {
-            int n = wn * 32 + nt * 16 + rrow;
-            float bv = bq[n0 + n];
-            #pragma unroll
-            for (int i = 0; i < 4; ++i) {
-                int m = m0 + wm * 32 + mt * 16 + quad * 4 + i;
-                q[(size_t)m * 128 + n0 + n] = __float2bfloat16(acc[mt][nt][i] + bv);
-            }
-        }
-    }
-}
-
-__global__ __launch_bounds__(256) void attn_mfma_kernel(
-    const __hip_bfloat16* __restrict__ q, const __hip_bfloat16* __restrict__ kvf,
-    const u64* __restrict__ maskbits, __hip_bfloat16* __restrict__ att)
-{
-    constexpr int RP = 208;
-    constexpr int QS = 40;
-    constexpr int VS = 232;
-    __shared__ short Qs[RP * QS];
-    __shared__ short Ks[RP * QS];
-    __shared__ short Vt[16 * VS];
-    __shared__ short Ps[4][16 * VS];
-    __shared__ u64 smask[RP][4];
-
-    int b = blockIdx.x >> 3, h = blockIdx.x & 7;
-    int half = blockIdx.y;
-    int t = threadIdx.x;
-    int wave = t >> 6, lane = t & 63;
-    int rrow = lane & 15, quad = lane >> 4;
-
-    const short8 z8 = {0, 0, 0, 0, 0, 0, 0, 0};
-    for (int idx = t; idx < RP * 2; idx += 256) {
-        int r = idx >> 1, g = idx & 1;
-        short8 qa = z8, ka = z8;
-        if (r < Rc) {
-            qa = *(const short8*)((const short*)q + ((size_t)(b * Rc + r)) * 128 + h * 16 + g * 8);
-            ka = *(const short8*)((const short*)kvf + ((size_t)(b * Nc + r)) * 256 + h * 16 + g * 8);
-        }
-        *(short8*)&Qs[r * QS + g * 8] = qa;
-        *(short8*)&Ks[r * QS + g * 8] = ka;
-        *(short8*)&Qs[r * QS + 16 + g * 8] = z8;
-        *(short8*)&Ks[r * QS + 16 + g * 8] = z8;
-    }
-    if (t < Rc) {
-        const short* vp = (const short*)kvf + ((size_t)(b * Nc + t)) * 256 + 128 + h * 16;
-        short8 v0 = *(const short8*)vp;
-        short8 v1 = *(const short8*)(vp + 8);
-        #pragma unroll
-        for (int d = 0; d < 8; ++d) Vt[d * VS + t] = v0[d];
-        #pragma unroll
-        for (int d = 0; d < 8; ++d) Vt[(d + 8) * VS + t] = v1[d];
-    }
-    for (int idx = t; idx < 16 * 32; idx += 256) {
-        int d = idx >> 5, cN = 200 + (idx & 31);
-        if (cN < VS) Vt[d * VS + cN] = 0;
-    }
-    for (int idx = lane; idx < 16 * 16; idx += 64) {
-        int rr = idx >> 4, cc = 208 + (idx & 15);
-        Ps[wave][rr * VS + cc] = 0;
-    }
-    for (int idx = t; idx < RP * 4; idx += 256) {
-        int r = idx >> 2, w = idx & 3;
-        smask[r][w] = (r < Rc) ? maskbits[((size_t)b * Rc + r) * 4 + w] : ~0ull;
-    }
-    __syncthreads();
-
-    int rt0 = half * 7, rt1 = half ? 13 : 7;
-    for (int rt = rt0 + wave; rt < rt1; rt += 4) {
-        short8 qf = *(const short8*)&Qs[(rt * 16 + rrow) * QS + quad * 8];
-        f32x4 sacc[13];
-        #pragma unroll
-        for (int nt = 0; nt < 13; ++nt) {
-            short8 kf = *(const short8*)&Ks[(nt * 16 + rrow) * QS + quad * 8];
-            sacc[nt] = __builtin_amdgcn_mfma_f32_16x16x32_bf16(
-                qf, kf, (f32x4){0.f, 0.f, 0.f, 0.f}, 0, 0, 0);
-        }
-        float inv[4];
+        for (int nt = 0; nt < 13; ++nt)
+            #pragma unroll
+            for (int kc = 0; kc < 4; ++kc) {
+                short8 bfr = *(const short8*)
+                    (Bsl + kc * 208 * 32 + (nt * 16 + rrow) * 32 + ((quad + srd) & 3) * 8);
+                acc[nt] = __builtin_amdgcn_mfma_f32_16x16x32_bf16(afr[kc], bfr, acc[nt], 0, 0, 0);
+            }
+
+        const float scale = 0.08838834764831843f;
         #pragma unroll
         for (int i = 0; i < 4; ++i) {
-            int r = rt * 16 + quad * 4 + i;
-            u64 wv0 = smask[r][0], wv1 = smask[r][1], wv2 = smask[r][2], wv3 = smask[r][3];
+            int rloc = wave * 16 + quad * 4 + i;
+            int r = m0 + rloc;
+            u64 w0 = sm[rloc * 4 + 0], w1 = sm[rloc * 4 + 1];
+            u64 w2 = sm[rloc * 4 + 2], w3 = sm[rloc * 4 + 3];
+            float vals[13];
             float mx = -INFINITY;
             #pragma unroll
             for (int nt = 0; nt < 13; ++nt) {
-                u64 w = (nt < 4) ? wv0 : (nt < 8) ? wv1 : (nt < 12) ? wv2 : wv3;
+                u64 w = (nt < 4) ? w0 : (nt < 8) ? w1 : (nt < 12) ? w2 : w3;
                 int sh = ((nt & 3) << 4) + rrow;
-                float s = ((w >> sh) & 1ull) ? sacc[nt][i] : -INFINITY;
-                sacc[nt][i] = s;
-                mx = fmaxf(mx, s);
+                float lg = ((w >> sh) & 1ull)
+                         ? 10.f * tanhf((acc[nt][i] + sbe[nt * 16 + rrow]) * scale)
+                         : -INFINITY;
+                vals[nt] = lg;
+                mx = fmaxf(mx, lg);
             }
             mx = fmaxf(mx, __shfl_xor(mx, 1));
             mx = fmaxf(mx, __shfl_xor(mx, 2));
@@ -502,130 +600,22 @@
             float l = 0.f;
             #pragma unroll
             for (int nt = 0; nt < 13; ++nt) {
-                float p = __expf(sacc[nt][i] - mx);
-                sacc[nt][i] = p;
+                float p = (vals[nt] == -INFINITY) ? 0.f : __expf(vals[nt] - mx);
+                vals[nt] = p;
                 l += p;
             }
             l += __shfl_xor(l, 1);
             l += __shfl_xor(l, 2);
             l += __shfl_xor(l, 4);
             l += __shfl_xor(l, 8);
-            inv[i] = (l > 0.f) ? 1.f / l : 0.f;
-        }
-        #pragma unroll
-        for (int nt = 0; nt < 13; ++nt)
-            #pragma unroll
-            for (int i = 0; i < 4; ++i)
-                *(__hip_bfloat16*)&Ps[wave][(quad * 4 + i) * VS + nt * 16 + rrow] =
-                    __float2bfloat16(sacc[nt][i]);
-        f32x4 oacc = (f32x4){0.f, 0.f, 0.f, 0.f};
-        #pragma unroll
-        for (int kt = 0; kt < 7; ++kt) {
-            short8 pf = *(const short8*)&Ps[wave][rrow * VS + kt * 32 + quad * 8];
-            short8 vf = *(const short8*)&Vt[rrow * VS + kt * 32 + quad * 8];
-            oacc = __builtin_amdgcn_mfma_f32_16x16x32_bf16(pf, vf, oacc, 0, 0, 0);
-        }
-        #pragma unroll
-        for (int i = 0; i < 4; ++i) {
-            int r = rt * 16 + quad * 4 + i;
-            if (r < Rc)
-                att[((size_t)(b * Rc + r)) * 128 + h * 16 + rrow] =
-                    __float2bfloat16(oacc[i] * inv[i]);
-        }
-    }
-}
-
-__global__ __launch_bounds__(128) void logits_softmax_kernel(
-    const __hip_bfloat16* __restrict__ att, const __hip_bfloat16* __restrict__ em,
-    const float* __restrict__ be, const u64* __restrict__ maskbits,
-    float* __restrict__ out)
-{
-    __shared__ short Asl[4][32 * 32];
-    __shared__ short Bsl[4][208 * 32];
-    __shared__ u64 sm[32][4];
-    __shared__ float sbe[208];
-    int b = blockIdx.x, m0 = blockIdx.y * 32;
-    int t = threadIdx.x, wave = t >> 6, lane = t & 63;
-    int lrow = lane >> 2, cg = lane & 3, ss = (lane >> 3) & 3, gq = (cg - ss) & 3;
-    int rrow = lane & 15, quad = lane >> 4, srd = (rrow >> 1) & 3;
-
-    const short* Aa = (const short*)att + ((size_t)b * Rc + m0) * 128;
-    const short* Ben = (const short*)em + (size_t)b * Nc * 128;
-
-    #pragma unroll
-    for (int kc = 0; kc < 4; ++kc)
-        GLOAD_LDS16(Aa + (size_t)(wave * 16 + lrow) * 128 + kc * 32 + gq * 8,
-                    &Asl[kc][(wave * 16) * 32]);
-    for (int cch = wave; cch < 13; cch += 2)
-        #pragma unroll
-        for (int kc = 0; kc < 4; ++kc)
-            GLOAD_LDS16(Ben + (size_t)(cch * 16 + lrow) * 128 + kc * 32 + gq * 8,
-                        &Bsl[kc][(cch * 16) * 32]);
-    {
-        int r = t >> 2, w = t & 3;
-        sm[r][w] = (m0 + r < Rc) ? maskbits[((size_t)b * Rc + m0 + r) * 4 + w] : 0ull;
-    }
-    for (int i = t; i < 208; i += 128) sbe[i] = (i < Nc) ? be[(size_t)b * Nc + i] : 0.f;
-    __syncthreads();
-
-    short8 afr[4];
-    #pragma unroll
-    for (int kc = 0; kc < 4; ++kc)
-        afr[kc] = *(const short8*)&Asl[kc][(wave * 16 + rrow) * 32 + ((quad + srd) & 3) * 8];
-
-    f32x4 acc[13];
-    #pragma unroll
-    for (int nt = 0; nt < 13; ++nt)
-        acc[nt] = (f32x4){0.f, 0.f, 0.f, 0.f};
-    #pragma unroll
-    for (int nt = 0; nt < 13; ++nt)
-        #pragma unroll
-        for (int kc = 0; kc < 4; ++kc) {
-            short8 bfr = *(const short8*)
-                &Bsl[kc][(nt * 16 + rrow) * 32 + ((quad + srd) & 3) * 8];
-            acc[nt] = __builtin_amdgcn_mfma_f32_16x16x32_bf16(afr[kc], bfr, acc[nt], 0, 0, 0);
-        }
-
-    const float scale = 0.08838834764831843f;
-    #pragma unroll
-    for (int i = 0; i < 4; ++i) {
-        int rloc = wave * 16 + quad * 4 + i;
-        int r = m0 + rloc;
-        u64 w0 = sm[rloc][0], w1 = sm[rloc][1], w2 = sm[rloc][2], w3 = sm[rloc][3];
-        float vals[13];
-        float mx = -INFINITY;
-        #pragma unroll
-        for (int nt = 0; nt < 13; ++nt) {
-            u64 w = (nt < 4) ? w0 : (nt < 8) ? w1 : (nt < 12) ? w2 : w3;
-            int sh = ((nt & 3) << 4) + rrow;
-            float lg = ((w >> sh) & 1ull)
-                     ? 10.f * tanhf((acc[nt][i] + sbe[nt * 16 + rrow]) * scale)
-                     : -INFINITY;
-            vals[nt] = lg;
-            mx = fmaxf(mx, lg);
-        }
-        mx = fmaxf(mx, __shfl_xor(mx, 1));
-        mx = fmaxf(mx, __shfl_xor(mx, 2));
-        mx = fmaxf(mx, __shfl_xor(mx, 4));
-        mx = fmaxf(mx, __shfl_xor(mx, 8));
-        float l = 0.f;
-        #pragma unroll
-        for (int nt = 0; nt < 13; ++nt) {
-            float p = (vals[nt] == -INFINITY) ? 0.f : __expf(vals[nt] - mx);
-            vals[nt] = p;
-            l += p;
-        }
-        l += __shfl_xor(l, 1);
-        l += __shfl_xor(l, 2);
-        l += __shfl_xor(l, 4);
-        l += __shfl_xor(l, 8);
-        float inv = (l > 0.f) ? 1.f / l : 0.f;
-        if (r < Rc) {
-            #pragma unroll
-            for (int nt = 0; nt < 13; ++nt) {
-                int n = nt * 16 + rrow;
-                if (n < Nc)
-                    out[((size_t)b * Rc + r) * Nc + n] = vals[nt] * inv;
+            float inv = (l > 0.f) ? 1.f / l : 0.f;
+            if (r < Rc) {
+                #pragma unroll
+                for (int nt = 0; nt < 13; ++nt) {
+                    int n = nt * 16 + rrow;
+                    if (n < Nc)
+                        out[((size_t)b * Rc + r) * Nc + n] = vals[nt] * inv;
+                }
             }
         }
     }
@@ -653,6 +643,7 @@
     char* ws = (char*)d_ws;
     size_t off = 0;
     auto alloc = [&](size_t bytes) { char* p = ws + off; off += (bytes + 255) & ~(size_t)255; return p; };
+    unsigned* bar = (unsigned*)alloc(256);
     __hip_bfloat16* W1t  = (__hip_bfloat16*)alloc((size_t)640 * 1280 * 2);
     __hip_bfloat16* Wkvt = (__hip_bfloat16*)alloc((size_t)256 * 128 * 2);
     __hip_bfloat16* Wmb  = (__hip_bfloat16*)alloc((size_t)128 * 128 * 2);
@@ -668,12 +659,9 @@
     float* be = (float*)alloc((size_t)Bc * Nc * 4);
     u64* maskbits = (u64*)alloc((size_t)BRc * 4 * 8);
 
-    prep_knn_kernel<<<2530, 256, 0, stream>>>(
-        W1, W2, Wq, Wmhc, Wk, Wv, b2, enc, dist, mask, cur,
-        W1t, Wkvt, Wmb, Wcat, bq, encb, aoff, hq, maskbits);
-    fused_gemms_kernel<<<1625, 256, 0, stream>>>(
-        encb, aoff, W1t, b1, Wkvt, Wmb, bmhc, enc, hq, kvf, em, be);
-    qgemm_kernel<<<dim3(2, BRc / 64), 256, 0, stream>>>(hq, Wcat, bq, q);
-    attn_mfma_kernel<<<dim3(Bc * Hc, 2), 256, 0, stream>>>(q, kvf, maskbits, att);
-    logits_softmax_kernel<<<dim3(Bc, 7), 128, 0, stream>>>(att, em, be, maskbits, out);
+    hipMemsetAsync(bar, 0, 256, stream);
+    mega_kernel<<<GRID, 256, 0, stream>>>(
+        W1, W2, Wq, Wmhc, Wk, Wv, bmhc, b1, b2, enc, dist, mask, cur,
+        W1t, Wkvt, Wmb, Wcat, bq, encb, aoff, hq, q, kvf, att, em, be,
+        maskbits, out, bar);
 }
```
